# Performance work log

Measured on AMD Instinct MI355X. Metric: run time of the kernel, lower is better.

## Reference

```python
import jax, jax.numpy as jnp
import numpy as np

N, D, H = 1024, 256, 512


def _linear_init(key, fan_in, fan_out):
    kw, kb = jax.random.split(key)
    bound = 1.0 / np.sqrt(fan_in)
    w = jax.random.uniform(kw, (fan_in, fan_out), jnp.float32, -bound, bound)
    b = jax.random.uniform(kb, (fan_out,), jnp.float32, -bound, bound)
    return w, b


def setup_inputs() -> dict:
    key = jax.random.key(0)
    ks = jax.random.split(key, 8)
    domain_a = jax.random.normal(ks[0], (N, D), jnp.float32)
    domain_b = jax.random.normal(ks[1], (N, D), jnp.float32)
    mu_w0, mu_b0 = _linear_init(ks[2], D, H)
    mu_w1, mu_b1 = _linear_init(ks[3], H, H)
    mu_w2, mu_b2 = _linear_init(ks[4], H, D)
    lv_w0, lv_b0 = _linear_init(ks[5], D, H)
    lv_w1, lv_b1 = _linear_init(ks[6], H, H)
    lv_w2, lv_b2 = _linear_init(ks[7], H, D)
    return dict(domain_a=domain_a, domain_b=domain_b,
                mu_w0=mu_w0, mu_b0=mu_b0, mu_w1=mu_w1, mu_b1=mu_b1, mu_w2=mu_w2, mu_b2=mu_b2,
                lv_w0=lv_w0, lv_b0=lv_b0, lv_w1=lv_w1, lv_b1=lv_b1, lv_w2=lv_w2, lv_b2=lv_b2)


def _net(x, ws, bs, final_act):
    h = x
    for i in range(len(ws)):
        h = h @ ws[i] + bs[i]
        if i < len(ws) - 1:
            h = jax.nn.relu(h)
    return final_act(h)


def _l2norm(h):
    # L2NormEncoder == F.normalize(dim=-1), eps clamp like torch
    n = jnp.maximum(jnp.linalg.norm(h, axis=-1, keepdims=True), 1e-12)
    return h / n


def reference(domain_a, domain_b, mu_w0, mu_b0, mu_w1, mu_b1, mu_w2, mu_b2,
              lv_w0, lv_b0, lv_w1, lv_b1, lv_w2, lv_b2):
    mu_ws, mu_bs = [mu_w0, mu_w1, mu_w2], [mu_b0, mu_b1, mu_b2]
    lv_ws, lv_bs = [lv_w0, lv_w1, lv_w2], [lv_b0, lv_b1, lv_b2]

    # ---- embedding-model loss: prob-model params frozen (requires_grad=False) ----
    sg = jax.lax.stop_gradient
    mu = _net(domain_a, [sg(w) for w in mu_ws], [sg(b) for b in mu_bs], _l2norm)
    log_var = _net(domain_a, [sg(w) for w in lv_ws], [sg(b) for b in lv_bs], jnp.tanh)
    inv_var = jnp.exp(-log_var)                                  # [N, D]
    pos_probs = jnp.sum(-(domain_b - mu) ** 2 * inv_var - log_var, axis=-1)  # [N]
    # pairwise: [i, j, d] = b[j, d] - mu[i, d]; mean over j
    diff2_mean = jnp.mean((domain_b[None, :, :] - mu[:, None, :]) ** 2, axis=1)  # [N, D]
    neg_probs = jnp.sum(-diff2_mean * inv_var - log_var, axis=-1)  # [N]
    embed_model_loss = jnp.mean(pos_probs - neg_probs)

    # ---- prob-model loss: embeddings detached, params trainable ----
    a_d, b_d = sg(domain_a), sg(domain_b)
    mu2 = _net(a_d, mu_ws, mu_bs, _l2norm)
    lv2 = _net(a_d, lv_ws, lv_bs, jnp.tanh)
    prob_model_loss = jnp.mean(jnp.sum((b_d - mu2) ** 2 * jnp.exp(-lv2) + lv2, axis=-1))

    emb_coef, prob_coef = 1.0, 1.0
    loss = emb_coef * embed_model_loss + prob_coef * prob_model_loss
    return loss
```

## Files before the change

kernel.cpp:

```cpp
#include <hip/hip_runtime.h>
#include <hip/hip_fp16.h>

#define N_ROWS 1024
#define DIM 256
#define HID 512

typedef _Float16 half_t;
typedef __attribute__((ext_vector_type(4))) _Float16 half4v;
typedef __attribute__((ext_vector_type(8))) _Float16 half8v;
typedef __attribute__((ext_vector_type(16))) float f32x16;

struct Params {
    const float* a;
    const float* b;
    const float* w[6];
    const float* bias[6];
    unsigned* flags;
    float* acc;
    unsigned* done;
    float* ebsum;
    float* eb2sum;
    unsigned short* g_mu;
    half_t* wt[6];
    float* out;
};

__global__ __launch_bounds__(256) void prep_kernel(Params p) {
    const int y = blockIdx.y, bx = blockIdx.x, tid = threadIdx.x;

    if (y == 6) {
        if (bx >= 64) return;
        const int d = tid, r0 = bx * 16;
        float s = 0.f, s2 = 0.f;
        #pragma unroll
        for (int r = 0; r < 16; ++r) {
            float v = p.b[(r0 + r) * DIM + d];
            s += v; s2 = fmaf(v, v, s2);
        }
        atomicAdd(&p.ebsum[d], s);
        atomicAdd(&p.eb2sum[d], s2);
        return;
    }
    __shared__ float T[32][33];
    const float* src = p.w[y];
    half_t* dst = p.wt[y];
    const int K = (y < 2) ? DIM : HID;
    const int N = (y < 4) ? HID : DIM;
    const int C = K >> 5;
    const int tilesN = N >> 5;
    if (bx >= C * tilesN) return;
    const int tk = bx / tilesN, tn = bx % tilesN;

    {
        const int r = tid >> 3, c4 = (tid & 7) * 4;
        float4 v = *(const float4*)&src[(tk * 32 + r) * N + tn * 32 + c4];
        T[r][c4 + 0] = v.x; T[r][c4 + 1] = v.y; T[r][c4 + 2] = v.z; T[r][c4 + 3] = v.w;
    }
    __syncthreads();

    const int which = tid >> 7;
    const int lane64 = (tid >> 1) & 63;
    const int epart = tid & 1;
    const int hi = lane64 >> 5, lr = lane64 & 31;
    const int rbase = which * 16 + hi * 8 + epart * 4;
    half4v h;
    h[0] = (half_t)T[rbase + 0][lr];
    h[1] = (half_t)T[rbase + 1][lr];
    h[2] = (half_t)T[rbase + 2][lr];
    h[3] = (half_t)T[rbase + 3][lr];
    *(half4v*)&dst[((tn * C + tk) * 2 + which) * 512 + lane64 * 8 + epart * 4] = h;
}

template <int NC, int NT, int MODE>
__device__ __forceinline__ void gemm_layer(const half_t* __restrict__ Xin,
                                           const half_t* __restrict__ Wfrag,
                                           const float* __restrict__ bias,
                                           half_t* __restrict__ Xout,
                                           float* __restrict__ rawL,
                                           unsigned short* __restrict__ gmu,
                                           const int R0) {
    const int tid = threadIdx.x;
    const int w = tid >> 6, lane = tid & 63;
    const int lr = lane & 31, hi = lane >> 5;
    const int sa = (lr >> 3) & 3;
    const int aoff0 = lr * 40 + ((hi ^ sa) * 8);
    const int aoff1 = lr * 40 + (((hi + 2) ^ sa) * 8);
    constexpr int PFW = (NC < 6) ? NC : 6;

    const half_t* Wp[NT];
    #pragma unroll
    for (int ct = 0; ct < NT; ++ct)
        Wp[ct] = Wfrag + (w * NT + ct) * NC * 1024 + lane * 8;

    f32x16 acc[NT];
    #pragma unroll
    for (int ct = 0; ct < NT; ++ct)
        #pragma unroll
        for (int i = 0; i < 16; ++i) acc[ct][i] = 0.f;

    half8v wbuf[NT][6][2], abuf[2][2];
    #define ISSUE_W(ct, c)                                                     \
        do {                                                                   \
            wbuf[ct][(c) % 6][0] = *(const half8v*)(Wp[ct] + (c) * 1024);      \
            wbuf[ct][(c) % 6][1] = *(const half8v*)(Wp[ct] + (c) * 1024 + 512);\
        } while (0)
    #define ISSUE_A(c)                                                         \
        do {                                                                   \
            abuf[(c) & 1][0] = *(const half8v*)&Xin[(c) * 1280 + aoff0];       \
            abuf[(c) & 1][1] = *(const half8v*)&Xin[(c) * 1280 + aoff1];       \
        } while (0)

    #pragma unroll
    for (int c = 0; c < PFW; ++c) {
        #pragma unroll
        for (int ct = 0; ct < NT; ++ct) ISSUE_W(ct, c);
    }
    ISSUE_A(0);
    if (NC > 1) ISSUE_A(1);

    #pragma unroll
    for (int c = 0; c < NC; ++c) {
        half8v av0 = abuf[c & 1][0], av1 = abuf[c & 1][1];
        if (c + 2 < NC) ISSUE_A(c + 2);
        #pragma unroll
        for (int ct = 0; ct < NT; ++ct) {
            half8v bv0 = wbuf[ct][c % 6][0], bv1 = wbuf[ct][c % 6][1];
            if (c + PFW < NC) ISSUE_W(ct, c + PFW);
            acc[ct] = __builtin_amdgcn_mfma_f32_32x32x16_f16(av0, bv0, acc[ct], 0, 0, 0);
            acc[ct] = __builtin_amdgcn_mfma_f32_32x32x16_f16(av1, bv1, acc[ct], 0, 0, 0);
        }
    }
    #undef ISSUE_W
    #undef ISSUE_A

    #pragma unroll
    for (int ct = 0; ct < NT; ++ct) {
        const int col0 = (w * NT + ct) * 32;
        const int col = col0 + lr;
        const float bv = bias[col];
        #pragma unroll
        for (int r = 0; r < 16; ++r) {
            const int row = (r & 3) + 8 * (r >> 2) + 4 * hi;
            float v = acc[ct][r] + bv;
            if (MODE == 0) {
                v = fmaxf(v, 0.f);
                const int kbp = (lr >> 3) ^ ((row >> 3) & 3);
                Xout[(col0 >> 5) * 1280 + row * 40 + kbp * 8 + (lr & 7)] = (half_t)v;
            } else if (MODE == 1) {
                union { half_t h; unsigned short u; } cv;
                cv.h = (half_t)v;
                __hip_atomic_store(&gmu[(R0 + row) * DIM + col], cv.u,
                                   __ATOMIC_RELAXED, __HIP_MEMORY_SCOPE_AGENT);
            } else {
                rawL[row * 256 + col] = v;
            }
        }
    }
}

__global__ void __launch_bounds__(512) main_kernel(Params p) {
    __shared__ alignas(16) char smem[81984];
    half_t* XA = (half_t*)smem;
    half_t* XB = (half_t*)(smem + 40960);
    float* rawL = (float*)(smem + 40960);
    float* bsum = (float*)(smem + 81920);

    const int bid = blockIdx.x, tid = threadIdx.x;
    const int net = bid & 1, g = bid >> 1, R0 = g * 32;

    {
        const int r = tid >> 4, q = tid & 15;
        const float* src = &p.a[(R0 + r) * DIM + q * 16];
        float4 v0 = *(const float4*)(src);
        float4 v1 = *(const float4*)(src + 4);
        float4 v2 = *(const float4*)(src + 8);
        float4 v3 = *(const float4*)(src + 12);
        half8v h0, h1;
        h0[0] = (half_t)v0.x; h0[1] = (half_t)v0.y; h0[2] = (half_t)v0.z; h0[3] = (half_t)v0.w;
        h0[4] = (half_t)v1.x; h0[5] = (half_t)v1.y; h0[6] = (half_t)v1.z; h0[7] = (half_t)v1.w;
        h1[0] = (half_t)v2.x; h1[1] = (half_t)v2.y; h1[2] = (half_t)v2.z; h1[3] = (half_t)v2.w;
        h1[4] = (half_t)v3.x; h1[5] = (half_t)v3.y; h1[6] = (half_t)v3.z; h1[7] = (half_t)v3.w;
        const int c = q >> 1, kb0 = (q & 1) * 2, s = (r >> 3) & 3;
        *(half8v*)&XA[c * 1280 + r * 40 + ((kb0 ^ s) * 8)] = h0;
        *(half8v*)&XA[c * 1280 + r * 40 + (((kb0 + 1) ^ s) * 8)] = h1;
    }
    __syncthreads();

    gemm_layer<8, 2, 0>(XA, p.wt[net], p.bias[net], XB, nullptr, nullptr, R0);
    __syncthreads();
    gemm_layer<16, 2, 0>(XB, p.wt[2 + net], p.bias[2 + net], XA, nullptr, nullptr, R0);
    __syncthreads();

    if (net == 0) {
        gemm_layer<16, 1, 1>(XA, p.wt[4], p.bias[4], nullptr, nullptr, p.g_mu, R0);
        asm volatile("s_waitcnt vmcnt(0)" ::: "memory");
        __syncthreads();
        if (tid == 0)
            __hip_atomic_store(&p.flags[g], 1u, __ATOMIC_RELAXED, __HIP_MEMORY_SCOPE_AGENT);
        return;
    }

    gemm_layer<16, 1, 2>(XA, p.wt[5], p.bias[5], nullptr, rawL, nullptr, R0);
    if (tid == 0) *bsum = 0.f;
    if (tid == 0) {
        while (__hip_atomic_load(&p.flags[g], __ATOMIC_RELAXED, __HIP_MEMORY_SCOPE_AGENT) == 0u)
            __builtin_amdgcn_s_sleep(1);
    }
    __syncthreads();
    asm volatile("" ::: "memory");

    const int wave = tid >> 6, lane = tid & 63;
    const float invN = 1.0f / (float)N_ROWS;
    float ebv[4], eb2v[4];
    #pragma unroll
    for (int t = 0; t < 4; ++t) {
        const int d = lane + t * 64;
        ebv[t]  = p.ebsum[d] * invN;
        eb2v[t] = p.eb2sum[d] * invN;
    }
    float wacc = 0.f;
    #pragma unroll
    for (int rr = 0; rr < 4; ++rr) {
        const int i = wave * 4 + rr;
        float m4[4], l4[4], ss = 0.f;
        #pragma unroll
        for (int t = 0; t < 4; ++t) {
            const int d = lane + t * 64;
            unsigned short mu_u = __hip_atomic_load(&p.g_mu[(R0 + i) * DIM + d],
                                                    __ATOMIC_RELAXED, __HIP_MEMORY_SCOPE_AGENT);
            union { unsigned short u; half_t h; } cv;
            cv.u = mu_u;
            m4[t] = (float)cv.h;
            l4[t] = rawL[i * 256 + d];
            ss = fmaf(m4[t], m4[t], ss);
        }
        #pragma unroll
        for (int o = 32; o > 0; o >>= 1) ss += __shfl_xor(ss, o, 64);
        const float inv_norm = 1.f / fmaxf(sqrtf(ss), 1e-12f);
        #pragma unroll
        for (int t = 0; t < 4; ++t) {
            float mu = m4[t] * inv_norm;
            float lv = tanhf(l4[t]);
            float iv = expf(-lv);
            float diff2 = fmaf(mu, mu, fmaf(-2.f * mu, ebv[t], eb2v[t]));
            wacc += fmaf(diff2, iv, lv);
        }
    }
    #pragma unroll
    for (int o = 32; o > 0; o >>= 1) wacc += __shfl_xor(wacc, o, 64);
    if (lane == 0) atomicAdd(bsum, wacc);
    __syncthreads();
    if (tid == 0) {
        atomicAdd(p.acc, *bsum);
        asm volatile("s_waitcnt vmcnt(0)" ::: "memory");
        unsigned prev = __hip_atomic_fetch_add(p.done, 1u, __ATOMIC_RELAXED,
                                               __HIP_MEMORY_SCOPE_AGENT);
        if (prev == 31u) {
            float v = __hip_atomic_load(p.acc, __ATOMIC_RELAXED, __HIP_MEMORY_SCOPE_AGENT);
            p.out[0] = v * (1.0f / (float)N_ROWS);
        }
    }
}

extern "C" void kernel_launch(void* const* d_in, const int* in_sizes, int n_in,
                              void* d_out, int out_size, void* d_ws, size_t ws_size,
                              hipStream_t stream) {
    Params p;
    p.a = (const float*)d_in[0];
    p.b = (const float*)d_in[1];
    p.w[0] = (const float*)d_in[2];  p.bias[0] = (const float*)d_in[3];
    p.w[2] = (const float*)d_in[4];  p.bias[2] = (const float*)d_in[5];
    p.w[4] = (const float*)d_in[6];  p.bias[4] = (const float*)d_in[7];
    p.w[1] = (const float*)d_in[8];  p.bias[1] = (const float*)d_in[9];
    p.w[3] = (const float*)d_in[10]; p.bias[3] = (const float*)d_in[11];
    p.w[5] = (const float*)d_in[12]; p.bias[5] = (const float*)d_in[13];

    float* f = (float*)d_ws;
    p.flags  = (unsigned*)f;
    p.acc    = f + 32;
    p.done   = (unsigned*)(f + 33);
    p.ebsum  = f + 64;
    p.eb2sum = f + 320;
    p.g_mu   = (unsigned short*)(f + 1024);
    half_t* hb = (half_t*)(p.g_mu + N_ROWS * DIM);
    p.wt[0] = hb;  hb += HID * DIM;
    p.wt[1] = hb;  hb += HID * DIM;
    p.wt[2] = hb;  hb += HID * HID;
    p.wt[3] = hb;  hb += HID * HID;
    p.wt[4] = hb;  hb += DIM * HID;
    p.wt[5] = hb;  hb += DIM * HID;
    p.out   = (float*)d_out;

    hipMemsetAsync(d_ws, 0, 4096, stream);
    prep_kernel<<<dim3(256, 7), 256, 0, stream>>>(p);
    main_kernel<<<64, 512, 0, stream>>>(p);
}
```

Baseline: 33.90 us.

## Split each MLP layer across four blocks with split-K and global flag sync

Grows main_kernel from 64 to 256 blocks. Each row-group/network pair is now split four ways over output column tiles, and each layer uses split-K across waves with an LDS reduction. Intermediate activations go through global memory, and blocks wait on per-group counters between layers. This raises parallelism across the GPU's CUs but adds global round-trips, spin-waits and smaller, unpipelined GEMM tiles, and it relies on all 256 blocks being co-resident.

```diff
diff --git a/kernel.cpp b/kernel.cpp
--- a/kernel.cpp
+++ b/kernel.cpp
@@ -4,6 +4,7 @@
 #define N_ROWS 1024
 #define DIM 256
 #define HID 512
+#define CTR 16
 
 typedef _Float16 half_t;
 typedef __attribute__((ext_vector_type(4))) _Float16 half4v;
@@ -15,12 +16,17 @@
     const float* b;
     const float* w[6];
     const float* bias[6];
-    unsigned* flags;
+    unsigned* c1;
+    unsigned* c2;
+    unsigned* c3;
     float* acc;
     unsigned* done;
     float* ebsum;
     float* eb2sum;
     unsigned short* g_mu;
+    unsigned short* g_lv;
+    half_t* g_h1[2];
+    half_t* g_h2[2];
     half_t* wt[6];
     float* out;
 };
@@ -57,7 +63,6 @@
         T[r][c4 + 0] = v.x; T[r][c4 + 1] = v.y; T[r][c4 + 2] = v.z; T[r][c4 + 3] = v.w;
     }
     __syncthreads();
-
     const int which = tid >> 7;
     const int lane64 = (tid >> 1) & 63;
     const int epart = tid & 1;
@@ -71,180 +76,218 @@
     *(half4v*)&dst[((tn * C + tk) * 2 + which) * 512 + lane64 * 8 + epart * 4] = h;
 }
 
-template <int NC, int NT, int MODE>
-__device__ __forceinline__ void gemm_layer(const half_t* __restrict__ Xin,
+__device__ __forceinline__ void flag_add(unsigned* c) {
+    asm volatile("s_waitcnt vmcnt(0)" ::: "memory");
+    __syncthreads();
+    if (threadIdx.x == 0)
+        __hip_atomic_fetch_add(c, 1u, __ATOMIC_RELAXED, __HIP_MEMORY_SCOPE_AGENT);
+}
+__device__ __forceinline__ void flag_wait(unsigned* c, unsigned tgt) {
+    if (threadIdx.x == 0) {
+        while (__hip_atomic_load(c, __ATOMIC_RELAXED, __HIP_MEMORY_SCOPE_AGENT) < tgt)
+            __builtin_amdgcn_s_sleep(1);
+    }
+    __syncthreads();
+    asm volatile("" ::: "memory");
+}
+
+template <int KC>
+__device__ __forceinline__ f32x16 mma_tile(const half_t* __restrict__ XA,
                                            const half_t* __restrict__ Wfrag,
-                                           const float* __restrict__ bias,
-                                           half_t* __restrict__ Xout,
-                                           float* __restrict__ rawL,
-                                           unsigned short* __restrict__ gmu,
-                                           const int R0) {
-    const int tid = threadIdx.x;
-    const int w = tid >> 6, lane = tid & 63;
+                                           const int NCtot, const int tile,
+                                           const int k0, const int lane) {
     const int lr = lane & 31, hi = lane >> 5;
     const int sa = (lr >> 3) & 3;
     const int aoff0 = lr * 40 + ((hi ^ sa) * 8);
     const int aoff1 = lr * 40 + (((hi + 2) ^ sa) * 8);
-    constexpr int PFW = (NC < 6) ? NC : 6;
-
-    const half_t* Wp[NT];
-    #pragma unroll
-    for (int ct = 0; ct < NT; ++ct)
-        Wp[ct] = Wfrag + (w * NT + ct) * NC * 1024 + lane * 8;
-
-    f32x16 acc[NT];
-    #pragma unroll
-    for (int ct = 0; ct < NT; ++ct)
-        #pragma unroll
-        for (int i = 0; i < 16; ++i) acc[ct][i] = 0.f;
-
-    half8v wbuf[NT][6][2], abuf[2][2];
-    #define ISSUE_W(ct, c)                                                     \
-        do {                                                                   \
-            wbuf[ct][(c) % 6][0] = *(const half8v*)(Wp[ct] + (c) * 1024);      \
-            wbuf[ct][(c) % 6][1] = *(const half8v*)(Wp[ct] + (c) * 1024 + 512);\
-        } while (0)
-    #define ISSUE_A(c)                                                         \
-        do {                                                                   \
-            abuf[(c) & 1][0] = *(const half8v*)&Xin[(c) * 1280 + aoff0];       \
-            abuf[(c) & 1][1] = *(const half8v*)&Xin[(c) * 1280 + aoff1];       \
-        } while (0)
-
-    #pragma unroll
-    for (int c = 0; c < PFW; ++c) {
-        #pragma unroll
-        for (int ct = 0; ct < NT; ++ct) ISSUE_W(ct, c);
-    }
-    ISSUE_A(0);
-    if (NC > 1) ISSUE_A(1);
-
-    #pragma unroll
-    for (int c = 0; c < NC; ++c) {
-        half8v av0 = abuf[c & 1][0], av1 = abuf[c & 1][1];
-        if (c + 2 < NC) ISSUE_A(c + 2);
-        #pragma unroll
-        for (int ct = 0; ct < NT; ++ct) {
-            half8v bv0 = wbuf[ct][c % 6][0], bv1 = wbuf[ct][c % 6][1];
-            if (c + PFW < NC) ISSUE_W(ct, c + PFW);
-            acc[ct] = __builtin_amdgcn_mfma_f32_32x32x16_f16(av0, bv0, acc[ct], 0, 0, 0);
-            acc[ct] = __builtin_amdgcn_mfma_f32_32x32x16_f16(av1, bv1, acc[ct], 0, 0, 0);
-        }
-    }
-    #undef ISSUE_W
-    #undef ISSUE_A
-
-    #pragma unroll
-    for (int ct = 0; ct < NT; ++ct) {
-        const int col0 = (w * NT + ct) * 32;
+    const half_t* Wp = Wfrag + (tile * NCtot + k0) * 1024 + lane * 8;
+    const half_t* Ap = XA + k0 * 1280;
+    f32x16 acc;
+    #pragma unroll
+    for (int i = 0; i < 16; ++i) acc[i] = 0.f;
+    #pragma unroll
+    for (int c = 0; c < KC; ++c) {
+        half8v av0 = *(const half8v*)&Ap[c * 1280 + aoff0];
+        half8v av1 = *(const half8v*)&Ap[c * 1280 + aoff1];
+        half8v bv0 = *(const half8v*)(Wp + c * 1024);
+        half8v bv1 = *(const half8v*)(Wp + c * 1024 + 512);
+        acc = __builtin_amdgcn_mfma_f32_32x32x16_f16(av0, bv0, acc, 0, 0, 0);
+        acc = __builtin_amdgcn_mfma_f32_32x32x16_f16(av1, bv1, acc, 0, 0, 0);
+    }
+    return acc;
+}
+
+__device__ __forceinline__ void stage_a(const float* __restrict__ a, half_t* XA,
+                                        const int R0, const int tid) {
+    const int r = tid >> 4, q = tid & 15;
+    const float* src = &a[(R0 + r) * DIM + q * 16];
+    float4 v0 = *(const float4*)(src);
+    float4 v1 = *(const float4*)(src + 4);
+    float4 v2 = *(const float4*)(src + 8);
+    float4 v3 = *(const float4*)(src + 12);
+    half8v h0, h1;
+    h0[0] = (half_t)v0.x; h0[1] = (half_t)v0.y; h0[2] = (half_t)v0.z; h0[3] = (half_t)v0.w;
+    h0[4] = (half_t)v1.x; h0[5] = (half_t)v1.y; h0[6] = (half_t)v1.z; h0[7] = (half_t)v1.w;
+    h1[0] = (half_t)v2.x; h1[1] = (half_t)v2.y; h1[2] = (half_t)v2.z; h1[3] = (half_t)v2.w;
+    h1[4] = (half_t)v3.x; h1[5] = (half_t)v3.y; h1[6] = (half_t)v3.z; h1[7] = (half_t)v3.w;
+    const int c = q >> 1, kb0 = (q & 1) * 2, sr = (r >> 3) & 3;
+    *(half8v*)&XA[c * 1280 + r * 40 + ((kb0 ^ sr) * 8)] = h0;
+    *(half8v*)&XA[c * 1280 + r * 40 + (((kb0 + 1) ^ sr) * 8)] = h1;
+}
+
+__device__ __forceinline__ void stage_h(const half_t* __restrict__ src, half_t* XA,
+                                        const int R0, const int tid) {
+    const int r = tid >> 4, q = tid & 15;
+    const half_t* sp = &src[(R0 + r) * HID + q * 32];
+    half8v x0 = *(const half8v*)(sp);
+    half8v x1 = *(const half8v*)(sp + 8);
+    half8v x2 = *(const half8v*)(sp + 16);
+    half8v x3 = *(const half8v*)(sp + 24);
+    const int sr = (r >> 3) & 3;
+    half_t* d = &XA[q * 1280 + r * 40];
+    *(half8v*)&d[(0 ^ sr) * 8] = x0;
+    *(half8v*)&d[(1 ^ sr) * 8] = x1;
+    *(half8v*)&d[(2 ^ sr) * 8] = x2;
+    *(half8v*)&d[(3 ^ sr) * 8] = x3;
+}
+
+__device__ __forceinline__ void reduce2_store(f32x16 acc, float* red,
+                                              const int tl, const int kh, const int lane,
+                                              const float* __restrict__ bias, const int col0,
+                                              unsigned short* __restrict__ dstG, const int Nout,
+                                              const int R0, const bool relu) {
+    __syncthreads();
+    if (kh) {
+        #pragma unroll
+        for (int i = 0; i < 16; ++i) red[tl * 1024 + i * 64 + lane] = acc[i];
+    }
+    __syncthreads();
+    if (!kh) {
+        const int lr = lane & 31, hi = lane >> 5;
         const int col = col0 + lr;
         const float bv = bias[col];
         #pragma unroll
-        for (int r = 0; r < 16; ++r) {
-            const int row = (r & 3) + 8 * (r >> 2) + 4 * hi;
-            float v = acc[ct][r] + bv;
-            if (MODE == 0) {
-                v = fmaxf(v, 0.f);
-                const int kbp = (lr >> 3) ^ ((row >> 3) & 3);
-                Xout[(col0 >> 5) * 1280 + row * 40 + kbp * 8 + (lr & 7)] = (half_t)v;
-            } else if (MODE == 1) {
-                union { half_t h; unsigned short u; } cv;
-                cv.h = (half_t)v;
-                __hip_atomic_store(&gmu[(R0 + row) * DIM + col], cv.u,
-                                   __ATOMIC_RELAXED, __HIP_MEMORY_SCOPE_AGENT);
-            } else {
-                rawL[row * 256 + col] = v;
-            }
+        for (int i = 0; i < 16; ++i) {
+            float v = acc[i] + red[tl * 1024 + i * 64 + lane] + bv;
+            if (relu) v = fmaxf(v, 0.f);
+            const int row = (i & 3) + 8 * (i >> 2) + 4 * hi;
+            union { half_t h; unsigned short u; } cv; cv.h = (half_t)v;
+            __hip_atomic_store(&dstG[(R0 + row) * Nout + col], cv.u,
+                               __ATOMIC_RELAXED, __HIP_MEMORY_SCOPE_AGENT);
         }
     }
 }
 
-__global__ void __launch_bounds__(512) main_kernel(Params p) {
-    __shared__ alignas(16) char smem[81984];
+__device__ __forceinline__ void reduce4_store(f32x16 acc, float* red,
+                                              const int tl, const int kq, const int lane,
+                                              const float* __restrict__ bias, const int col0,
+                                              unsigned short* __restrict__ dstG, const int Nout,
+                                              const int R0) {
+    __syncthreads();
+    if (kq) {
+        #pragma unroll
+        for (int i = 0; i < 16; ++i)
+            red[(tl * 3 + kq - 1) * 1024 + i * 64 + lane] = acc[i];
+    }
+    __syncthreads();
+    if (!kq) {
+        const int lr = lane & 31, hi = lane >> 5;
+        const int col = col0 + lr;
+        const float bv = bias[col];
+        #pragma unroll
+        for (int i = 0; i < 16; ++i) {
+            float v = acc[i] + bv
+                    + red[(tl * 3 + 0) * 1024 + i * 64 + lane]
+                    + red[(tl * 3 + 1) * 1024 + i * 64 + lane]
+                    + red[(tl * 3 + 2) * 1024 + i * 64 + lane];
+            const int row = (i & 3) + 8 * (i >> 2) + 4 * hi;
+            union { half_t h; unsigned short u; } cv; cv.h = (half_t)v;
+            __hip_atomic_store(&dstG[(R0 + row) * Nout + col], cv.u,
+                               __ATOMIC_RELAXED, __HIP_MEMORY_SCOPE_AGENT);
+        }
+    }
+}
+
+__global__ void __launch_bounds__(512, 2) main_kernel(Params p) {
+    __shared__ alignas(16) char smem[41024];
     half_t* XA = (half_t*)smem;
-    half_t* XB = (half_t*)(smem + 40960);
-    float* rawL = (float*)(smem + 40960);
-    float* bsum = (float*)(smem + 81920);
+    float* red = (float*)smem;
+    float* bsum = (float*)(smem + 40960);
 
     const int bid = blockIdx.x, tid = threadIdx.x;
-    const int net = bid & 1, g = bid >> 1, R0 = g * 32;
-
+    const int net = bid & 1, g = (bid >> 1) & 31, s = bid >> 6;
+    const int R0 = g * 32;
+    const int w = tid >> 6, lane = tid & 63;
+
+    stage_a(p.a, XA, R0, tid);
+    __syncthreads();
     {
-        const int r = tid >> 4, q = tid & 15;
-        const float* src = &p.a[(R0 + r) * DIM + q * 16];
-        float4 v0 = *(const float4*)(src);
-        float4 v1 = *(const float4*)(src + 4);
-        float4 v2 = *(const float4*)(src + 8);
-        float4 v3 = *(const float4*)(src + 12);
-        half8v h0, h1;
-        h0[0] = (half_t)v0.x; h0[1] = (half_t)v0.y; h0[2] = (half_t)v0.z; h0[3] = (half_t)v0.w;
-        h0[4] = (half_t)v1.x; h0[5] = (half_t)v1.y; h0[6] = (half_t)v1.z; h0[7] = (half_t)v1.w;
-        h1[0] = (half_t)v2.x; h1[1] = (half_t)v2.y; h1[2] = (half_t)v2.z; h1[3] = (half_t)v2.w;
-        h1[4] = (half_t)v3.x; h1[5] = (half_t)v3.y; h1[6] = (half_t)v3.z; h1[7] = (half_t)v3.w;
-        const int c = q >> 1, kb0 = (q & 1) * 2, s = (r >> 3) & 3;
-        *(half8v*)&XA[c * 1280 + r * 40 + ((kb0 ^ s) * 8)] = h0;
-        *(half8v*)&XA[c * 1280 + r * 40 + (((kb0 + 1) ^ s) * 8)] = h1;
-    }
-    __syncthreads();
-
-    gemm_layer<8, 2, 0>(XA, p.wt[net], p.bias[net], XB, nullptr, nullptr, R0);
-    __syncthreads();
-    gemm_layer<16, 2, 0>(XB, p.wt[2 + net], p.bias[2 + net], XA, nullptr, nullptr, R0);
-    __syncthreads();
-
-    if (net == 0) {
-        gemm_layer<16, 1, 1>(XA, p.wt[4], p.bias[4], nullptr, nullptr, p.g_mu, R0);
-        asm volatile("s_waitcnt vmcnt(0)" ::: "memory");
-        __syncthreads();
-        if (tid == 0)
-            __hip_atomic_store(&p.flags[g], 1u, __ATOMIC_RELAXED, __HIP_MEMORY_SCOPE_AGENT);
-        return;
-    }
-
-    gemm_layer<16, 1, 2>(XA, p.wt[5], p.bias[5], nullptr, rawL, nullptr, R0);
+        const int tl = w >> 1, kh = w & 1;
+        const int tile = s * 4 + tl;
+        f32x16 acc = mma_tile<4>(XA, p.wt[net], 8, tile, kh * 4, lane);
+        reduce2_store(acc, red, tl, kh, lane, p.bias[net], tile * 32,
+                      (unsigned short*)p.g_h1[net], HID, R0, true);
+    }
+    flag_add(p.c1 + (net * 32 + g) * CTR);
+
+    flag_wait(p.c1 + (net * 32 + g) * CTR, 4);
+    stage_h(p.g_h1[net], XA, R0, tid);
+    __syncthreads();
+    {
+        const int tl = w >> 1, kh = w & 1;
+        const int tile = s * 4 + tl;
+        f32x16 acc = mma_tile<8>(XA, p.wt[2 + net], 16, tile, kh * 8, lane);
+        reduce2_store(acc, red, tl, kh, lane, p.bias[2 + net], tile * 32,
+                      (unsigned short*)p.g_h2[net], HID, R0, true);
+    }
+    flag_add(p.c2 + (net * 32 + g) * CTR);
+
+    flag_wait(p.c2 + (net * 32 + g) * CTR, 4);
+    stage_h(p.g_h2[net], XA, R0, tid);
+    __syncthreads();
+    {
+        const int tl = w >> 2, kq = w & 3;
+        const int tile = s * 2 + tl;
+        f32x16 acc = mma_tile<4>(XA, p.wt[4 + net], 16, tile, kq * 4, lane);
+        reduce4_store(acc, red, tl, kq, lane, p.bias[4 + net], tile * 32,
+                      net ? p.g_lv : p.g_mu, DIM, R0);
+    }
+    flag_add(p.c3 + g * CTR);
+
+    if (net == 0) return;
+
     if (tid == 0) *bsum = 0.f;
-    if (tid == 0) {
-        while (__hip_atomic_load(&p.flags[g], __ATOMIC_RELAXED, __HIP_MEMORY_SCOPE_AGENT) == 0u)
-            __builtin_amdgcn_s_sleep(1);
-    }
-    __syncthreads();
-    asm volatile("" ::: "memory");
-
-    const int wave = tid >> 6, lane = tid & 63;
+    flag_wait(p.c3 + g * CTR, 8);
+
+    const int i = R0 + s * 8 + w;
+    const int d0 = lane * 4;
+    const half_t* muP = (const half_t*)p.g_mu;
+    const half_t* lvP = (const half_t*)p.g_lv;
+    half4v mh = *(const half4v*)&muP[i * DIM + d0];
+    half4v lh = *(const half4v*)&lvP[i * DIM + d0];
+    float4 ebf = *(const float4*)&p.ebsum[d0];
+    float4 eb2f = *(const float4*)&p.eb2sum[d0];
     const float invN = 1.0f / (float)N_ROWS;
-    float ebv[4], eb2v[4];
+    float m4[4] = {(float)mh[0], (float)mh[1], (float)mh[2], (float)mh[3]};
+    float l4[4] = {(float)lh[0], (float)lh[1], (float)lh[2], (float)lh[3]};
+    float eb[4] = {ebf.x * invN, ebf.y * invN, ebf.z * invN, ebf.w * invN};
+    float eb2[4] = {eb2f.x * invN, eb2f.y * invN, eb2f.z * invN, eb2f.w * invN};
+
+    float ss = 0.f;
+    #pragma unroll
+    for (int t = 0; t < 4; ++t) ss = fmaf(m4[t], m4[t], ss);
+    #pragma unroll
+    for (int o = 32; o > 0; o >>= 1) ss += __shfl_xor(ss, o, 64);
+    const float inv_norm = 1.f / fmaxf(sqrtf(ss), 1e-12f);
+
+    float wacc = 0.f;
     #pragma unroll
     for (int t = 0; t < 4; ++t) {
-        const int d = lane + t * 64;
-        ebv[t]  = p.ebsum[d] * invN;
-        eb2v[t] = p.eb2sum[d] * invN;
-    }
-    float wacc = 0.f;
-    #pragma unroll
-    for (int rr = 0; rr < 4; ++rr) {
-        const int i = wave * 4 + rr;
-        float m4[4], l4[4], ss = 0.f;
-        #pragma unroll
-        for (int t = 0; t < 4; ++t) {
-            const int d = lane + t * 64;
-            unsigned short mu_u = __hip_atomic_load(&p.g_mu[(R0 + i) * DIM + d],
-                                                    __ATOMIC_RELAXED, __HIP_MEMORY_SCOPE_AGENT);
-            union { unsigned short u; half_t h; } cv;
-            cv.u = mu_u;
-            m4[t] = (float)cv.h;
-            l4[t] = rawL[i * 256 + d];
-            ss = fmaf(m4[t], m4[t], ss);
-        }
-        #pragma unroll
-        for (int o = 32; o > 0; o >>= 1) ss += __shfl_xor(ss, o, 64);
-        const float inv_norm = 1.f / fmaxf(sqrtf(ss), 1e-12f);
-        #pragma unroll
-        for (int t = 0; t < 4; ++t) {
-            float mu = m4[t] * inv_norm;
-            float lv = tanhf(l4[t]);
-            float iv = expf(-lv);
-            float diff2 = fmaf(mu, mu, fmaf(-2.f * mu, ebv[t], eb2v[t]));
-            wacc += fmaf(diff2, iv, lv);
-        }
+        float mu = m4[t] * inv_norm;
+        float lv = tanhf(l4[t]);
+        float iv = expf(-lv);
+        float diff2 = fmaf(mu, mu, fmaf(-2.f * mu, eb[t], eb2[t]));
+        wacc += fmaf(diff2, iv, lv);
     }
     #pragma unroll
     for (int o = 32; o > 0; o >>= 1) wacc += __shfl_xor(wacc, o, 64);
@@ -255,7 +298,7 @@
         asm volatile("s_waitcnt vmcnt(0)" ::: "memory");
         unsigned prev = __hip_atomic_fetch_add(p.done, 1u, __ATOMIC_RELAXED,
                                                __HIP_MEMORY_SCOPE_AGENT);
-        if (prev == 31u) {
+        if (prev == 127u) {
             float v = __hip_atomic_load(p.acc, __ATOMIC_RELAXED, __HIP_MEMORY_SCOPE_AGENT);
             p.out[0] = v * (1.0f / (float)N_ROWS);
         }
@@ -276,22 +319,29 @@
     p.w[5] = (const float*)d_in[12]; p.bias[5] = (const float*)d_in[13];
 
     float* f = (float*)d_ws;
-    p.flags  = (unsigned*)f;
-    p.acc    = f + 32;
-    p.done   = (unsigned*)(f + 33);
-    p.ebsum  = f + 64;
-    p.eb2sum = f + 320;
-    p.g_mu   = (unsigned short*)(f + 1024);
-    half_t* hb = (half_t*)(p.g_mu + N_ROWS * DIM);
+    p.c1   = (unsigned*)f;
+    p.c2   = (unsigned*)(f + 1024);
+    p.c3   = (unsigned*)(f + 2048);
+    p.acc  = f + 2560;
+    p.done = (unsigned*)(f + 2576);
+    p.ebsum  = f + 2816;
+    p.eb2sum = f + 3072;
+    p.g_mu = (unsigned short*)(f + 4096);
+    p.g_lv = (unsigned short*)(f + 4096 + 65536 * 2);
+    half_t* hb = (half_t*)(f + 4096 + 65536 * 4);
+    p.g_h1[0] = hb;  hb += N_ROWS * HID;
+    p.g_h1[1] = hb;  hb += N_ROWS * HID;
+    p.g_h2[0] = hb;  hb += N_ROWS * HID;
+    p.g_h2[1] = hb;  hb += N_ROWS * HID;
     p.wt[0] = hb;  hb += HID * DIM;
     p.wt[1] = hb;  hb += HID * DIM;
     p.wt[2] = hb;  hb += HID * HID;
     p.wt[3] = hb;  hb += HID * HID;
     p.wt[4] = hb;  hb += DIM * HID;
     p.wt[5] = hb;  hb += DIM * HID;
-    p.out   = (float*)d_out;
-
-    hipMemsetAsync(d_ws, 0, 4096, stream);
+    p.out = (float*)d_out;
+
+    hipMemsetAsync(d_ws, 0, 16384, stream);
     prep_kernel<<<dim3(256, 7), 256, 0, stream>>>(p);
-    main_kernel<<<64, 512, 0, stream>>>(p);
-}
+    main_kernel<<<256, 512, 0, stream>>>(p);
+}
```

New measurement: 31.17 us. -8.1%, faster.
